# Kernel tuning notes

Hardware: AMD Instinct MI355X
Metric: run time of the kernel (lower is better)

The kernel has to match this reference:

```python
import jax, jax.numpy as jnp
import numpy as np

B, S = 4, 4096
D_MODEL = 1024
INDEXER_DIM = 64
LOCAL_WINDOW = 16
MEDIUM_WINDOW = 64
GLOBAL_K = 32
LOCAL_SPARSE = 0.8


def _local_k_schedule(seq_len):
    # Replicates torch: k_local = max(1, int(L * (1 - local_sparse))) with Python float math
    ks = []
    for q in range(seq_len):
        L = min(q + 1, LOCAL_WINDOW)
        ks.append(max(1, int(L * (1.0 - LOCAL_SPARSE))))
    ks = np.asarray(ks, dtype=np.int32)
    return ks, int(ks.max())


def setup_inputs() -> dict:
    key = jax.random.key(0)
    kx, kl, km, kg = jax.random.split(key, 4)
    scale = D_MODEL ** -0.5
    return {
        "x": jax.random.normal(kx, (B, S, D_MODEL), jnp.float32),
        "W_local": jax.random.normal(kl, (INDEXER_DIM, D_MODEL), jnp.float32) * scale,
        "W_medium": jax.random.normal(km, (INDEXER_DIM, D_MODEL), jnp.float32) * scale,
        "W_global": jax.random.normal(kg, (INDEXER_DIM, D_MODEL), jnp.float32) * scale,
    }


def reference(x, W_local, W_medium, W_global):
    Bb, Ss, _ = x.shape
    neg_inf = jnp.array(-jnp.inf, x.dtype)
    zero = jnp.array(0.0, x.dtype)

    lf = x @ W_local.T   # [B,S,i]
    mf = x @ W_medium.T  # computed by the original but DEAD: medium branch never fires
    gf = x @ W_global.T  # [B,S,i]

    mask = jnp.full((Bb, 1, Ss, Ss), -jnp.inf, x.dtype)
    q_ix = jnp.arange(Ss)
    b_ix = jnp.arange(Bb)[:, None, None]
    qq = q_ix[None, :, None]

    # ---- local scale: causal window [max(0, q-W+1), q] ----
    offs = jnp.arange(LOCAL_WINDOW)
    win = q_ix[:, None] - (LOCAL_WINDOW - 1) + offs[None, :]  # [S,W] absolute key positions
    valid = win >= 0
    winc = jnp.clip(win, 0, Ss - 1)
    lwin = lf[:, winc]                                        # [B,S,W,i]
    lscores = jax.nn.relu(jnp.einsum('bqd,bqwd->bqw', lf, lwin))
    lscores = jnp.where(valid[None], lscores, -jnp.inf)
    ks, kmax = _local_k_schedule(Ss)
    _, tl = jax.lax.top_k(lscores, kmax)                      # [B,S,kmax] window-relative
    labs = jnp.take_along_axis(jnp.broadcast_to(winc[None], (Bb, Ss, LOCAL_WINDOW)), tl, axis=-1)
    keep = jnp.arange(kmax)[None, None, :] < jnp.asarray(ks)[None, :, None]  # [1,S,kmax]
    lvals = jnp.where(keep, zero, neg_inf)
    mask = mask.at[b_ix, 0, qq, labs].max(jnp.broadcast_to(lvals, labs.shape))

    # ---- medium scale: DEAD CODE in the original (medium_end == local_end always) ----

    # ---- global scale (active because seq_len > medium_window and global_k > 0) ----
    if Ss > MEDIUM_WINDOW and GLOBAL_K > 0:
        gs = jax.nn.relu(jnp.einsum('bqd,bkd->bqk', gf, gf))  # [B,S,S]
        j = jnp.arange(Ss)[None, :]
        banned = (j <= q_ix[:, None]) & (j >= q_ix[:, None] - (LOCAL_WINDOW - 1))  # [S,S]
        gs = jnp.where(banned[None], -jnp.inf, gs)
        _, tg = jax.lax.top_k(gs, GLOBAL_K)                   # [B,S,Kg]
        mask = mask.at[b_ix, 0, qq, tg].max(jnp.zeros(tg.shape, x.dtype))

    return mask
```

## Files before the change

kernel.cpp:

```cpp
#include <hip/hip_runtime.h>
#include <hip/hip_fp16.h>
#include <cstdint>

#define SEQ 4096
#define NB 4
#define DMODEL 1024
#define ID 64
#define LW 16
#define GK 32
#define TQ 4

#define NEG_INF (-__builtin_inff())
#define MASKED4 0xFBFFFBFFu

__device__ __forceinline__ float2 h2f2(unsigned int u) {
    __half2 h = *reinterpret_cast<__half2*>(&u);
    return __half22float2(h);
}

__global__ __launch_bounds__(256)
void hp_feat_v7(const unsigned short* __restrict__ x,
                const unsigned short* __restrict__ Wl,
                const unsigned short* __restrict__ Wg,
                float* __restrict__ lf, float* __restrict__ gfT)
{
    __shared__ float xs[32][68];
    __shared__ float ws[32][68];
    __shared__ float trans[64][68];

    const int tid = threadIdx.x;
    const int half = blockIdx.x & 1;
    const long row0 = (long)(blockIdx.x >> 1) * 64;
    const unsigned short* W = half ? Wg : Wl;
    const int tx = tid & 15, ty = tid >> 4;

    float acc[4][4];
#pragma unroll
    for (int r = 0; r < 4; r++)
#pragma unroll
        for (int c = 0; c < 4; c++) acc[r][c] = 0.f;

    for (int k0 = 0; k0 < DMODEL; k0 += 32) {
        {
            int r = tid >> 2, c8 = (tid & 3) * 8;
            uint4 v = *(const uint4*)(x + (row0 + r) * DMODEL + k0 + c8);
            float2 f;
            f = h2f2(v.x); xs[c8 + 0][r] = f.x; xs[c8 + 1][r] = f.y;
            f = h2f2(v.y); xs[c8 + 2][r] = f.x; xs[c8 + 3][r] = f.y;
            f = h2f2(v.z); xs[c8 + 4][r] = f.x; xs[c8 + 5][r] = f.y;
            f = h2f2(v.w); xs[c8 + 6][r] = f.x; xs[c8 + 7][r] = f.y;
        }
        {
            int r = tid >> 2, c8 = (tid & 3) * 8;
            uint4 v = *(const uint4*)(W + (long)r * DMODEL + k0 + c8);
            float2 f;
            f = h2f2(v.x); ws[c8 + 0][r] = f.x; ws[c8 + 1][r] = f.y;
            f = h2f2(v.y); ws[c8 + 2][r] = f.x; ws[c8 + 3][r] = f.y;
            f = h2f2(v.z); ws[c8 + 4][r] = f.x; ws[c8 + 5][r] = f.y;
            f = h2f2(v.w); ws[c8 + 6][r] = f.x; ws[c8 + 7][r] = f.y;
        }
        __syncthreads();
#pragma unroll
        for (int kk = 0; kk < 32; kk++) {
            float4 a  = *(const float4*)&xs[kk][ty * 4];
            float4 bv = *(const float4*)&ws[kk][tx * 4];
            const float ar[4] = {a.x, a.y, a.z, a.w};
            const float bc[4] = {bv.x, bv.y, bv.z, bv.w};
#pragma unroll
            for (int r = 0; r < 4; r++)
#pragma unroll
                for (int c = 0; c < 4; c++)
                    acc[r][c] = fmaf(ar[r], bc[c], acc[r][c]);
        }
        __syncthreads();
    }

    if (!half) {
#pragma unroll
        for (int r = 0; r < 4; r++) {
            float4 st = make_float4(acc[r][0], acc[r][1], acc[r][2], acc[r][3]);
            *(float4*)(lf + (row0 + ty * 4 + r) * ID + tx * 4) = st;
        }
    } else {
#pragma unroll
        for (int r = 0; r < 4; r++)
#pragma unroll
            for (int c = 0; c < 4; c++)
                trans[tx * 4 + c][ty * 4 + r] = acc[r][c];
        __syncthreads();
        const int b = (int)(row0 >> 12), s0 = (int)(row0 & 4095);
        const int col = tid >> 2, rs = (tid & 3) * 16;
        float* dst = gfT + ((long)b * ID + col) * SEQ + s0 + rs;
#pragma unroll
        for (int u = 0; u < 4; u++)
            *(float4*)(dst + 4 * u) = *(const float4*)&trans[col][rs + 4 * u];
    }
}

__global__ __launch_bounds__(256)
void hp_mask_v8(const float* __restrict__ lf, const float* __restrict__ gfT,
                unsigned short* __restrict__ out)
{
    __shared__ float qv[TQ][ID];
    __shared__ float lq[TQ][ID];
    __shared__ unsigned long long red[4][4];
    __shared__ unsigned int bitmap[TQ][SEQ / 32];
    __shared__ float lsc[TQ][LW];
    __shared__ unsigned short tm[256];

    const int tid = threadIdx.x;
    const int lane = tid & 63, w = tid >> 6;
    const int bq = blockIdx.x;
    const int b = bq >> 10;
    const int q0 = (bq & 1023) * TQ;
    const float* gTb = gfT + (long)b * ID * SEQ;
    const float* lfb = lf + (long)b * SEQ * ID;

    {
        int d = tid >> 2, qi = tid & 3;
        qv[qi][d] = gTb[(long)d * SEQ + q0 + qi];
        int qi2 = tid >> 6, d2 = tid & 63;
        lq[qi2][d2] = lfb[(long)(q0 + qi2) * ID + d2];
        ((unsigned int*)bitmap)[tid] = 0u;
        ((unsigned int*)bitmap)[tid + 256] = 0u;
    }
    __syncthreads();

    float acc[4][4][TQ];
#pragma unroll
    for (int c = 0; c < 4; c++)
#pragma unroll
        for (int j = 0; j < 4; j++)
#pragma unroll
            for (int qi = 0; qi < TQ; qi++) acc[c][j][qi] = 0.f;

    for (int d = 0; d < ID; d++) {
        float qd[TQ];
#pragma unroll
        for (int qi = 0; qi < TQ; qi++) qd[qi] = qv[qi][d];
        const float4* rowp = (const float4*)(gTb + (long)d * SEQ);
#pragma unroll
        for (int c = 0; c < 4; c++) {
            float4 kv = rowp[c * 256 + tid];
#pragma unroll
            for (int qi = 0; qi < TQ; qi++) {
                acc[c][0][qi] = fmaf(kv.x, qd[qi], acc[c][0][qi]);
                acc[c][1][qi] = fmaf(kv.y, qd[qi], acc[c][1][qi]);
                acc[c][2][qi] = fmaf(kv.z, qd[qi], acc[c][2][qi]);
                acc[c][3][qi] = fmaf(kv.w, qd[qi], acc[c][3][qi]);
            }
        }
    }

    unsigned int uv[4][4][TQ];
#pragma unroll
    for (int c = 0; c < 4; c++)
#pragma unroll
        for (int j = 0; j < 4; j++) {
            const int k = 1024 * c + 4 * tid + j;
#pragma unroll
            for (int qi = 0; qi < TQ; qi++) {
                const int q = q0 + qi;
                const bool banned = (k <= q) && (k >= q - (LW - 1));
                uv[c][j][qi] = banned ? 0u
                    : (__float_as_uint(fmaxf(acc[c][j][qi], 0.f)) + 1u);
            }
        }

    unsigned int lo[TQ], hi[TQ];
#pragma unroll
    for (int qi = 0; qi < TQ; qi++) { lo[qi] = 0u; hi[qi] = 0xFFFFFFFFu; }

#pragma unroll 1
    for (int it = 0; it < 32; ++it) {
        unsigned int mid[TQ];
        unsigned long long pc = 0ull;
#pragma unroll
        for (int qi = 0; qi < TQ; qi++) {
            mid[qi] = lo[qi] + ((hi[qi] - lo[qi]) >> 1);
            int cnt = 0;
#pragma unroll
            for (int c = 0; c < 4; c++)
#pragma unroll
                for (int j = 0; j < 4; j++)
                    cnt += __popcll(__ballot(uv[c][j][qi] >= mid[qi]));
            pc |= (unsigned long long)(unsigned int)cnt << (16 * qi);
        }
        if (lane == 0) red[it & 1][w] = pc;
        __syncthreads();
        const unsigned long long tot = red[it & 1][0] + red[it & 1][1]
                                     + red[it & 1][2] + red[it & 1][3];
#pragma unroll
        for (int qi = 0; qi < TQ; qi++) {
            const unsigned int cnt =
                (unsigned int)((tot >> (16 * qi)) & 0xFFFFull);
            if (cnt >= GK) lo[qi] = mid[qi]; else hi[qi] = mid[qi];
        }
    }

    int C1[TQ], T[TQ], need[TQ];
    {
        unsigned long long pg = 0ull, pe = 0ull;
#pragma unroll
        for (int qi = 0; qi < TQ; qi++) {
            int cg = 0, ce = 0;
#pragma unroll
            for (int c = 0; c < 4; c++)
#pragma unroll
                for (int j = 0; j < 4; j++) {
                    const unsigned int v = uv[c][j][qi];
                    cg += __popcll(__ballot(v > lo[qi]));
                    ce += __popcll(__ballot(v == lo[qi]));
                }
            pg |= (unsigned long long)(unsigned int)cg << (16 * qi);
            pe |= (unsigned long long)(unsigned int)ce << (16 * qi);
        }
        if (lane == 0) { red[2][w] = pg; red[3][w] = pe; }
        __syncthreads();
        const unsigned long long tg = red[2][0] + red[2][1] + red[2][2] + red[2][3];
        const unsigned long long te = red[3][0] + red[3][1] + red[3][2] + red[3][3];
#pragma unroll
        for (int qi = 0; qi < TQ; qi++) {
            C1[qi]   = (int)((tg >> (16 * qi)) & 0xFFFFull);
            T[qi]    = (int)((te >> (16 * qi)) & 0xFFFFull);
            need[qi] = GK - C1[qi];
        }
    }

#pragma unroll
    for (int qi = 0; qi < TQ; qi++) {
        const bool allties = (T[qi] == need[qi]);
#pragma unroll
        for (int c = 0; c < 4; c++)
#pragma unroll
            for (int j = 0; j < 4; j++) {
                const unsigned int v = uv[c][j][qi];
                const bool sel_ = (v > lo[qi]) | (allties & (v == lo[qi]));
                if (sel_) {
                    const int k = 1024 * c + 4 * tid + j;
                    atomicOr(&bitmap[qi][k >> 5], 1u << (k & 31));
                }
            }
    }

#pragma unroll 1
    for (int qi = 0; qi < TQ; qi++) {
        if (T[qi] > need[qi]) {
            unsigned int m16 = 0u;
#pragma unroll
            for (int c = 0; c < 4; c++)
#pragma unroll
                for (int j = 0; j < 4; j++)
                    if (uv[c][j][qi] == lo[qi]) m16 |= 1u << (c * 4 + j);
            tm[tid] = (unsigned short)m16;
            __syncthreads();
            if (tid == 0) {
                int taken = 0;
                for (int c = 0; c < 4 && taken < need[qi]; c++)
                    for (int t = 0; t < 256 && taken < need[qi]; t++) {
                        const unsigned int nib = ((unsigned int)tm[t] >> (c * 4)) & 15u;
                        for (int j = 0; j < 4 && taken < need[qi]; j++)
                            if ((nib >> j) & 1u) {
                                const int k = 1024 * c + 4 * t + j;
                                atomicOr(&bitmap[qi][k >> 5], 1u << (k & 31));
                                taken++;
                            }
                    }
            }
            __syncthreads();
        }
    }

    if (tid < TQ * LW) {
        int qi = tid >> 4, wnd = tid & 15;
        int q = q0 + qi;
        int win = q - (LW - 1) + wnd;
        float v = NEG_INF;
        if (win >= 0) {
            const float4* kr = (const float4*)(lfb + (long)win * ID);
            float s = 0.f;
#pragma unroll
            for (int d = 0; d < 16; d++) {
                float4 kvv = kr[d];
                const float4 qd = *(const float4*)&lq[qi][d * 4];
                s = fmaf(kvv.x, qd.x, s); s = fmaf(kvv.y, qd.y, s);
                s = fmaf(kvv.z, qd.z, s); s = fmaf(kvv.w, qd.w, s);
            }
            v = fmaxf(s, 0.f);
        }
        lsc[qi][wnd] = v;
    }
    __syncthreads();
    if (tid < TQ) {
        int qi = tid, q = q0 + qi;
        int L = (q + 1 < LW) ? q + 1 : LW;
        int ks = L / 5; if (ks < 1) ks = 1;
        for (int t = 0; t < ks; t++) {
            float best = NEG_INF; int bi = 0;
            for (int wnd = 0; wnd < LW; wnd++) {
                float v = lsc[qi][wnd];
                if (v > best) { best = v; bi = wnd; }
            }
            lsc[qi][bi] = NEG_INF;
            const int win = q - (LW - 1) + bi;
            atomicOr(&bitmap[qi][win >> 5], 1u << (win & 31));
        }
    }
    __syncthreads();

    uint4* orow = (uint4*)(out + ((long)b * SEQ + q0) * SEQ);
#pragma unroll
    for (int i = 0; i < TQ * SEQ / 8 / 256; i++) {
        const int li = i * 256 + tid;
        const int qi = li >> 9;
        const int w8 = li & 511;
        const unsigned int bits =
            (bitmap[qi][w8 >> 2] >> ((w8 & 3) * 8)) & 0xFFu;
        uint4 v;
        v.x = MASKED4 & ~(((bits &   1u) ? 0x0000FFFFu : 0u) |
                          ((bits &   2u) ? 0xFFFF0000u : 0u));
        v.y = MASKED4 & ~(((bits &   4u) ? 0x0000FFFFu : 0u) |
                          ((bits &   8u) ? 0xFFFF0000u : 0u));
        v.z = MASKED4 & ~(((bits &  16u) ? 0x0000FFFFu : 0u) |
                          ((bits &  32u) ? 0xFFFF0000u : 0u));
        v.w = MASKED4 & ~(((bits &  64u) ? 0x0000FFFFu : 0u) |
                          ((bits & 128u) ? 0xFFFF0000u : 0u));
        orow[li] = v;
    }
}

extern "C" void kernel_launch(void* const* d_in, const int* in_sizes, int n_in,
                              void* d_out, int out_size, void* d_ws, size_t ws_size,
                              hipStream_t stream) {
    const unsigned short* x  = (const unsigned short*)d_in[0];
    const unsigned short* Wl = (const unsigned short*)d_in[1];
    const unsigned short* Wg = (const unsigned short*)d_in[3];
    unsigned short* out = (unsigned short*)d_out;

    float* lf  = (float*)d_ws;
    float* gfT = lf + (long)NB * SEQ * ID;

    hp_feat_v7<<<(NB * SEQ / 64) * 2, 256, 0, stream>>>(x, Wl, Wg, lf, gfT);
    hp_mask_v8<<<NB * SEQ / TQ, 256, 0, stream>>>(lf, gfT, out);
}
```

Before: 758.6 us.

## Use MFMA for feature projection and widen mask kernel to 512 threads

The feature projection kernel now issues 16x16x32 f16 MFMA instructions that read operands straight from global memory, replacing the LDS-staged fp32 FMA tiling. The mask kernel doubles its block to 512 threads, which halves per-thread score registers, and it runs the top-k radix bisection on float values in place. The bisection also exits early once every query's bounds have converged. Risks include uncoalesced global operand loads in the MFMA kernel, different rounding from f16 accumulation ordering, and more block-level reduction work across 8 waves.

New measurement: 753.5 us. Within noise of the previous version (-0.7%).

```diff
diff --git a/kernel.cpp b/kernel.cpp
--- a/kernel.cpp
+++ b/kernel.cpp
@@ -12,101 +12,71 @@
 
 #define NEG_INF (-__builtin_inff())
 #define MASKED4 0xFBFFFBFFu
-
-__device__ __forceinline__ float2 h2f2(unsigned int u) {
-    __half2 h = *reinterpret_cast<__half2*>(&u);
-    return __half22float2(h);
-}
+#define FMAT (NB * SEQ * ID)
+
+typedef _Float16 f16x8 __attribute__((ext_vector_type(8)));
+typedef float f32x4 __attribute__((ext_vector_type(4)));
 
 __global__ __launch_bounds__(256)
-void hp_feat_v7(const unsigned short* __restrict__ x,
-                const unsigned short* __restrict__ Wl,
-                const unsigned short* __restrict__ Wg,
-                float* __restrict__ lf, float* __restrict__ gfT)
+void hp_feat_v10(const unsigned short* __restrict__ xu,
+                 const unsigned short* __restrict__ Wlu,
+                 const unsigned short* __restrict__ Wgu,
+                 float* __restrict__ lf, float* __restrict__ gfT)
 {
-    __shared__ float xs[32][68];
-    __shared__ float ws[32][68];
-    __shared__ float trans[64][68];
-
     const int tid = threadIdx.x;
+    const int lane = tid & 63, w = tid >> 6;
     const int half = blockIdx.x & 1;
     const long row0 = (long)(blockIdx.x >> 1) * 64;
-    const unsigned short* W = half ? Wg : Wl;
-    const int tx = tid & 15, ty = tid >> 4;
-
-    float acc[4][4];
-#pragma unroll
-    for (int r = 0; r < 4; r++)
-#pragma unroll
-        for (int c = 0; c < 4; c++) acc[r][c] = 0.f;
-
+    const _Float16* xp = (const _Float16*)xu;
+    const _Float16* Wp = (const _Float16*)(half ? Wgu : Wlu);
+
+    const int lr = lane & 15;
+    const int kg = lane >> 4;
+
+    const _Float16* ap = xp + (row0 + w * 16 + lr) * DMODEL + kg * 8;
+    const _Float16* bp = Wp + (long)lr * DMODEL + kg * 8;
+
+    f32x4 acc[4];
+#pragma unroll
+    for (int ct = 0; ct < 4; ct++) acc[ct] = (f32x4){0.f, 0.f, 0.f, 0.f};
+
+#pragma unroll 4
     for (int k0 = 0; k0 < DMODEL; k0 += 32) {
-        {
-            int r = tid >> 2, c8 = (tid & 3) * 8;
-            uint4 v = *(const uint4*)(x + (row0 + r) * DMODEL + k0 + c8);
-            float2 f;
-            f = h2f2(v.x); xs[c8 + 0][r] = f.x; xs[c8 + 1][r] = f.y;
-            f = h2f2(v.y); xs[c8 + 2][r] = f.x; xs[c8 + 3][r] = f.y;
-            f = h2f2(v.z); xs[c8 + 4][r] = f.x; xs[c8 + 5][r] = f.y;
-            f = h2f2(v.w); xs[c8 + 6][r] = f.x; xs[c8 + 7][r] = f.y;
-        }
-        {
-            int r = tid >> 2, c8 = (tid & 3) * 8;
-            uint4 v = *(const uint4*)(W + (long)r * DMODEL + k0 + c8);
-            float2 f;
-            f = h2f2(v.x); ws[c8 + 0][r] = f.x; ws[c8 + 1][r] = f.y;
-            f = h2f2(v.y); ws[c8 + 2][r] = f.x; ws[c8 + 3][r] = f.y;
-            f = h2f2(v.z); ws[c8 + 4][r] = f.x; ws[c8 + 5][r] = f.y;
-            f = h2f2(v.w); ws[c8 + 6][r] = f.x; ws[c8 + 7][r] = f.y;
-        }
-        __syncthreads();
-#pragma unroll
-        for (int kk = 0; kk < 32; kk++) {
-            float4 a  = *(const float4*)&xs[kk][ty * 4];
-            float4 bv = *(const float4*)&ws[kk][tx * 4];
-            const float ar[4] = {a.x, a.y, a.z, a.w};
-            const float bc[4] = {bv.x, bv.y, bv.z, bv.w};
+        f16x8 av = *(const f16x8*)(ap + k0);
+#pragma unroll
+        for (int ct = 0; ct < 4; ct++) {
+            f16x8 bv = *(const f16x8*)(bp + (long)ct * 16 * DMODEL + k0);
+            acc[ct] = __builtin_amdgcn_mfma_f32_16x16x32_f16(av, bv, acc[ct], 0, 0, 0);
+        }
+    }
+
+    if (!half) {
+#pragma unroll
+        for (int ct = 0; ct < 4; ct++)
 #pragma unroll
             for (int r = 0; r < 4; r++)
-#pragma unroll
-                for (int c = 0; c < 4; c++)
-                    acc[r][c] = fmaf(ar[r], bc[c], acc[r][c]);
-        }
-        __syncthreads();
-    }
-
-    if (!half) {
-#pragma unroll
-        for (int r = 0; r < 4; r++) {
-            float4 st = make_float4(acc[r][0], acc[r][1], acc[r][2], acc[r][3]);
-            *(float4*)(lf + (row0 + ty * 4 + r) * ID + tx * 4) = st;
-        }
+                lf[(row0 + w * 16 + kg * 4 + r) * ID + ct * 16 + lr] = acc[ct][r];
     } else {
-#pragma unroll
-        for (int r = 0; r < 4; r++)
-#pragma unroll
-            for (int c = 0; c < 4; c++)
-                trans[tx * 4 + c][ty * 4 + r] = acc[r][c];
-        __syncthreads();
-        const int b = (int)(row0 >> 12), s0 = (int)(row0 & 4095);
-        const int col = tid >> 2, rs = (tid & 3) * 16;
-        float* dst = gfT + ((long)b * ID + col) * SEQ + s0 + rs;
-#pragma unroll
-        for (int u = 0; u < 4; u++)
-            *(float4*)(dst + 4 * u) = *(const float4*)&trans[col][rs + 4 * u];
+        const int bb = (int)(row0 >> 12), s0 = (int)(row0 & 4095);
+#pragma unroll
+        for (int ct = 0; ct < 4; ct++) {
+            float4 st = make_float4(acc[ct][0], acc[ct][1], acc[ct][2], acc[ct][3]);
+            *(float4*)(gfT + ((long)bb * ID + ct * 16 + lr) * SEQ
+                           + s0 + w * 16 + kg * 4) = st;
+        }
     }
 }
 
-__global__ __launch_bounds__(256)
-void hp_mask_v8(const float* __restrict__ lf, const float* __restrict__ gfT,
-                unsigned short* __restrict__ out)
+__global__ __launch_bounds__(512)
+void hp_mask_v10(const float* __restrict__ lf, const float* __restrict__ gfT,
+                 unsigned short* __restrict__ out)
 {
     __shared__ float qv[TQ][ID];
     __shared__ float lq[TQ][ID];
-    __shared__ unsigned long long red[4][4];
+    __shared__ unsigned long long red[4][8];
     __shared__ unsigned int bitmap[TQ][SEQ / 32];
     __shared__ float lsc[TQ][LW];
-    __shared__ unsigned short tm[256];
+    __shared__ unsigned short tm[512];
 
     const int tid = threadIdx.x;
     const int lane = tid & 63, w = tid >> 6;
@@ -116,128 +86,138 @@
     const float* gTb = gfT + (long)b * ID * SEQ;
     const float* lfb = lf + (long)b * SEQ * ID;
 
-    {
+    if (tid < 256) {
         int d = tid >> 2, qi = tid & 3;
         qv[qi][d] = gTb[(long)d * SEQ + q0 + qi];
         int qi2 = tid >> 6, d2 = tid & 63;
         lq[qi2][d2] = lfb[(long)(q0 + qi2) * ID + d2];
-        ((unsigned int*)bitmap)[tid] = 0u;
-        ((unsigned int*)bitmap)[tid + 256] = 0u;
-    }
+    }
+    ((unsigned int*)bitmap)[tid] = 0u;
     __syncthreads();
 
-    float acc[4][4][TQ];
-#pragma unroll
-    for (int c = 0; c < 4; c++)
+    float acc[2][4][TQ];
+#pragma unroll
+    for (int c = 0; c < 2; c++)
 #pragma unroll
         for (int j = 0; j < 4; j++)
 #pragma unroll
             for (int qi = 0; qi < TQ; qi++) acc[c][j][qi] = 0.f;
 
+    const float4* gT4 = (const float4*)gTb;
     for (int d = 0; d < ID; d++) {
         float qd[TQ];
 #pragma unroll
         for (int qi = 0; qi < TQ; qi++) qd[qi] = qv[qi][d];
-        const float4* rowp = (const float4*)(gTb + (long)d * SEQ);
-#pragma unroll
-        for (int c = 0; c < 4; c++) {
-            float4 kv = rowp[c * 256 + tid];
-#pragma unroll
-            for (int qi = 0; qi < TQ; qi++) {
-                acc[c][0][qi] = fmaf(kv.x, qd[qi], acc[c][0][qi]);
-                acc[c][1][qi] = fmaf(kv.y, qd[qi], acc[c][1][qi]);
-                acc[c][2][qi] = fmaf(kv.z, qd[qi], acc[c][2][qi]);
-                acc[c][3][qi] = fmaf(kv.w, qd[qi], acc[c][3][qi]);
-            }
-        }
-    }
-
-    unsigned int uv[4][4][TQ];
-#pragma unroll
-    for (int c = 0; c < 4; c++)
+        const float4 ka = gT4[(d << 10) + tid];
+        const float4 kb = gT4[(d << 10) + 512 + tid];
+#pragma unroll
+        for (int qi = 0; qi < TQ; qi++) {
+            acc[0][0][qi] = fmaf(ka.x, qd[qi], acc[0][0][qi]);
+            acc[0][1][qi] = fmaf(ka.y, qd[qi], acc[0][1][qi]);
+            acc[0][2][qi] = fmaf(ka.z, qd[qi], acc[0][2][qi]);
+            acc[0][3][qi] = fmaf(ka.w, qd[qi], acc[0][3][qi]);
+            acc[1][0][qi] = fmaf(kb.x, qd[qi], acc[1][0][qi]);
+            acc[1][1][qi] = fmaf(kb.y, qd[qi], acc[1][1][qi]);
+            acc[1][2][qi] = fmaf(kb.z, qd[qi], acc[1][2][qi]);
+            acc[1][3][qi] = fmaf(kb.w, qd[qi], acc[1][3][qi]);
+        }
+    }
+
+#pragma unroll
+    for (int c = 0; c < 2; c++)
 #pragma unroll
         for (int j = 0; j < 4; j++) {
-            const int k = 1024 * c + 4 * tid + j;
+            const int k = 2048 * c + 4 * tid + j;
 #pragma unroll
             for (int qi = 0; qi < TQ; qi++) {
                 const int q = q0 + qi;
                 const bool banned = (k <= q) && (k >= q - (LW - 1));
-                uv[c][j][qi] = banned ? 0u
-                    : (__float_as_uint(fmaxf(acc[c][j][qi], 0.f)) + 1u);
+                acc[c][j][qi] = banned ? -1.0f : fmaxf(acc[c][j][qi], 0.f);
             }
         }
 
     unsigned int lo[TQ], hi[TQ];
 #pragma unroll
-    for (int qi = 0; qi < TQ; qi++) { lo[qi] = 0u; hi[qi] = 0xFFFFFFFFu; }
+    for (int qi = 0; qi < TQ; qi++) { lo[qi] = 0u; hi[qi] = 0x7F800000u; }
 
 #pragma unroll 1
     for (int it = 0; it < 32; ++it) {
-        unsigned int mid[TQ];
         unsigned long long pc = 0ull;
 #pragma unroll
         for (int qi = 0; qi < TQ; qi++) {
-            mid[qi] = lo[qi] + ((hi[qi] - lo[qi]) >> 1);
+            const unsigned int mid = lo[qi] + ((hi[qi] - lo[qi]) >> 1);
+            const float tf = __uint_as_float(mid - 1u);
             int cnt = 0;
 #pragma unroll
-            for (int c = 0; c < 4; c++)
+            for (int c = 0; c < 2; c++)
 #pragma unroll
                 for (int j = 0; j < 4; j++)
-                    cnt += __popcll(__ballot(uv[c][j][qi] >= mid[qi]));
+                    cnt += __popcll(__ballot(acc[c][j][qi] >= tf));
             pc |= (unsigned long long)(unsigned int)cnt << (16 * qi);
         }
         if (lane == 0) red[it & 1][w] = pc;
         __syncthreads();
-        const unsigned long long tot = red[it & 1][0] + red[it & 1][1]
-                                     + red[it & 1][2] + red[it & 1][3];
-#pragma unroll
-        for (int qi = 0; qi < TQ; qi++) {
+        unsigned long long tot = 0ull;
+#pragma unroll
+        for (int ww = 0; ww < 8; ww++) tot += red[it & 1][ww];
+        int conv = 1;
+#pragma unroll
+        for (int qi = 0; qi < TQ; qi++) {
+            const unsigned int mid = lo[qi] + ((hi[qi] - lo[qi]) >> 1);
             const unsigned int cnt =
                 (unsigned int)((tot >> (16 * qi)) & 0xFFFFull);
-            if (cnt >= GK) lo[qi] = mid[qi]; else hi[qi] = mid[qi];
-        }
-    }
-
-    int C1[TQ], T[TQ], need[TQ];
+            if (cnt >= GK) lo[qi] = mid; else hi[qi] = mid;
+            conv &= (hi[qi] - lo[qi] <= 1u);
+        }
+        if (conv) break;
+    }
+
+    int T[TQ], need[TQ];
     {
         unsigned long long pg = 0ull, pe = 0ull;
 #pragma unroll
         for (int qi = 0; qi < TQ; qi++) {
+            const float tg = __uint_as_float(lo[qi]);
+            const unsigned int eb = lo[qi] - 1u;
             int cg = 0, ce = 0;
 #pragma unroll
-            for (int c = 0; c < 4; c++)
+            for (int c = 0; c < 2; c++)
 #pragma unroll
                 for (int j = 0; j < 4; j++) {
-                    const unsigned int v = uv[c][j][qi];
-                    cg += __popcll(__ballot(v > lo[qi]));
-                    ce += __popcll(__ballot(v == lo[qi]));
+                    const float v = acc[c][j][qi];
+                    cg += __popcll(__ballot(v >= tg));
+                    ce += __popcll(__ballot(__float_as_uint(v) == eb));
                 }
             pg |= (unsigned long long)(unsigned int)cg << (16 * qi);
             pe |= (unsigned long long)(unsigned int)ce << (16 * qi);
         }
         if (lane == 0) { red[2][w] = pg; red[3][w] = pe; }
         __syncthreads();
-        const unsigned long long tg = red[2][0] + red[2][1] + red[2][2] + red[2][3];
-        const unsigned long long te = red[3][0] + red[3][1] + red[3][2] + red[3][3];
-#pragma unroll
-        for (int qi = 0; qi < TQ; qi++) {
-            C1[qi]   = (int)((tg >> (16 * qi)) & 0xFFFFull);
+        unsigned long long tg = 0ull, te = 0ull;
+#pragma unroll
+        for (int ww = 0; ww < 8; ww++) { tg += red[2][ww]; te += red[3][ww]; }
+#pragma unroll
+        for (int qi = 0; qi < TQ; qi++) {
+            const int c1 = (int)((tg >> (16 * qi)) & 0xFFFFull);
             T[qi]    = (int)((te >> (16 * qi)) & 0xFFFFull);
-            need[qi] = GK - C1[qi];
+            need[qi] = GK - c1;
         }
     }
 
 #pragma unroll
     for (int qi = 0; qi < TQ; qi++) {
         const bool allties = (T[qi] == need[qi]);
-#pragma unroll
-        for (int c = 0; c < 4; c++)
+        const float tg = __uint_as_float(lo[qi]);
+        const unsigned int eb = lo[qi] - 1u;
+#pragma unroll
+        for (int c = 0; c < 2; c++)
 #pragma unroll
             for (int j = 0; j < 4; j++) {
-                const unsigned int v = uv[c][j][qi];
-                const bool sel_ = (v > lo[qi]) | (allties & (v == lo[qi]));
+                const float v = acc[c][j][qi];
+                const bool sel_ = (v >= tg)
+                                | (allties & (__float_as_uint(v) == eb));
                 if (sel_) {
-                    const int k = 1024 * c + 4 * tid + j;
+                    const int k = 2048 * c + 4 * tid + j;
                     atomicOr(&bitmap[qi][k >> 5], 1u << (k & 31));
                 }
             }
@@ -246,22 +226,24 @@
 #pragma unroll 1
     for (int qi = 0; qi < TQ; qi++) {
         if (T[qi] > need[qi]) {
+            const unsigned int eb = lo[qi] - 1u;
             unsigned int m16 = 0u;
 #pragma unroll
-            for (int c = 0; c < 4; c++)
+            for (int c = 0; c < 2; c++)
 #pragma unroll
                 for (int j = 0; j < 4; j++)
-                    if (uv[c][j][qi] == lo[qi]) m16 |= 1u << (c * 4 + j);
+                    if (__float_as_uint(acc[c][j][qi]) == eb)
+                        m16 |= 1u << (c * 4 + j);
             tm[tid] = (unsigned short)m16;
             __syncthreads();
             if (tid == 0) {
                 int taken = 0;
-                for (int c = 0; c < 4 && taken < need[qi]; c++)
-                    for (int t = 0; t < 256 && taken < need[qi]; t++) {
+                for (int c = 0; c < 2 && taken < need[qi]; c++)
+                    for (int t = 0; t < 512 && taken < need[qi]; t++) {
                         const unsigned int nib = ((unsigned int)tm[t] >> (c * 4)) & 15u;
                         for (int j = 0; j < 4 && taken < need[qi]; j++)
                             if ((nib >> j) & 1u) {
-                                const int k = 1024 * c + 4 * t + j;
+                                const int k = 2048 * c + 4 * t + j;
                                 atomicOr(&bitmap[qi][k >> 5], 1u << (k & 31));
                                 taken++;
                             }
@@ -310,8 +292,8 @@
 
     uint4* orow = (uint4*)(out + ((long)b * SEQ + q0) * SEQ);
 #pragma unroll
-    for (int i = 0; i < TQ * SEQ / 8 / 256; i++) {
-        const int li = i * 256 + tid;
+    for (int i = 0; i < TQ * SEQ / 8 / 512; i++) {
+        const int li = i * 512 + tid;
         const int qi = li >> 9;
         const int w8 = li & 511;
         const unsigned int bits =
@@ -338,8 +320,8 @@
     unsigned short* out = (unsigned short*)d_out;
 
     float* lf  = (float*)d_ws;
-    float* gfT = lf + (long)NB * SEQ * ID;
-
-    hp_feat_v7<<<(NB * SEQ / 64) * 2, 256, 0, stream>>>(x, Wl, Wg, lf, gfT);
-    hp_mask_v8<<<NB * SEQ / TQ, 256, 0, stream>>>(lf, gfT, out);
+    float* gfT = lf + (long)FMAT;
+
+    hp_feat_v10<<<(NB * SEQ / 64) * 2, 256, 0, stream>>>(x, Wl, Wg, lf, gfT);
+    hp_mask_v10<<<NB * SEQ / TQ, 512, 0, stream>>>(lf, gfT, out);
 }
```
